# Performance work log

Hardware: AMD Instinct MI355X
Metric: run time of the kernel (lower is better)

Reference implementation:

```python
import jax, jax.numpy as jnp
import numpy as np

D_MODEL = 1024
N_HEADS = 16
HEAD_DIM = D_MODEL // N_HEADS
THETA = 10000.0
B, S = 4, 2048


def setup_inputs() -> dict:
    key = jax.random.key(0)
    ks = jax.random.split(key, 5)
    scale = 1.0 / np.sqrt(D_MODEL)
    x = jax.random.normal(ks[0], (B, S, D_MODEL), dtype=jnp.float32)
    token_positions = jnp.broadcast_to(jnp.arange(S, dtype=jnp.int32)[None, :], (B, S))
    WQ = jax.random.normal(ks[1], (D_MODEL, D_MODEL), dtype=jnp.float32) * scale
    WK = jax.random.normal(ks[2], (D_MODEL, D_MODEL), dtype=jnp.float32) * scale
    WV = jax.random.normal(ks[3], (D_MODEL, D_MODEL), dtype=jnp.float32) * scale
    WO = jax.random.normal(ks[4], (D_MODEL, D_MODEL), dtype=jnp.float32) * scale
    return {"x": x, "token_positions": token_positions, "WQ": WQ, "WK": WK, "WV": WV, "WO": WO}


def _apply_rope(t, token_positions):
    # t: [b, h, s, d]; token_positions: [b, s]
    d = t.shape[-1]
    inv_freq = THETA ** (-jnp.arange(0, d, 2, dtype=jnp.float32) / d)  # [d/2]
    ang = token_positions.astype(jnp.float32)[:, None, :, None] * inv_freq  # [b,1,s,d/2]
    cos, sin = jnp.cos(ang), jnp.sin(ang)
    t_even, t_odd = t[..., 0::2], t[..., 1::2]
    r_even = t_even * cos - t_odd * sin
    r_odd = t_even * sin + t_odd * cos
    out = jnp.stack([r_even, r_odd], axis=-1)  # interleave pairs back
    return out.reshape(t.shape)


def reference(x, token_positions, WQ, WK, WV, WO):
    b, s, _ = x.shape
    def proj(W):
        y = jnp.einsum('bsd,ed->bse', x, W)  # Linear: x @ W^T, W is [out,in]
        return y.reshape(b, s, N_HEADS, HEAD_DIM).transpose(0, 2, 1, 3)  # [b,h,s,d]
    Q = _apply_rope(proj(WQ), token_positions)
    K = _apply_rope(proj(WK), token_positions)
    V = proj(WV)
    scores = jnp.einsum('bhqd,bhkd->bhqk', Q, K) / jnp.sqrt(jnp.float32(HEAD_DIM))
    causal = jnp.tril(jnp.ones((s, s), dtype=bool))
    scores = jnp.where(causal, scores, -jnp.inf)
    attn = jax.nn.softmax(scores, axis=-1)
    out = jnp.einsum('bhqk,bhkd->bhqd', attn, V)
    out = out.transpose(0, 2, 1, 3).reshape(b, s, D_MODEL)
    return jnp.einsum('bse,oe->bso', out, WO)
```

## Files before the change

kernel.cpp:

```cpp
#include <hip/hip_runtime.h>

typedef __bf16 bf16x8 __attribute__((ext_vector_type(8)));
typedef __bf16 bf16x2 __attribute__((ext_vector_type(2)));
typedef float f32x4 __attribute__((ext_vector_type(4)));
typedef unsigned short u16;
typedef unsigned int u32;

#define MFMA16(a, b, c) __builtin_amdgcn_mfma_f32_16x16x32_bf16((a), (b), (c), 0, 0, 0)

__device__ __forceinline__ u16 f2b(float f) {
  u32 u = __float_as_uint(f);
  u += 0x7FFFu + ((u >> 16) & 1u);
  return (u16)(u >> 16);
}
__device__ __forceinline__ float b2f(u16 h) { return __uint_as_float(((u32)h) << 16); }

__device__ __forceinline__ u32 pkbf(float a, float b) {
  bf16x2 h = {(__bf16)a, (__bf16)b};
  return __builtin_bit_cast(u32, h);
}

__device__ __forceinline__ float exp2_(float x) {
#if __has_builtin(__builtin_amdgcn_exp2f)
  return __builtin_amdgcn_exp2f(x);
#else
  return exp2f(x);
#endif
}

__device__ __forceinline__ void glds16(const void* g, void* l) {
  __builtin_amdgcn_global_load_lds((const __attribute__((address_space(1))) void*)g,
                                   (__attribute__((address_space(3))) void*)l, 16, 0, 0);
}

__global__ __launch_bounds__(256) void cvt_k(const float* __restrict__ x,
                                             const float* __restrict__ wq,
                                             const float* __restrict__ wk,
                                             const float* __restrict__ wv,
                                             const float* __restrict__ wo,
                                             u16* __restrict__ dst) {
  size_t e = ((size_t)blockIdx.x * 256 + threadIdx.x) * 4;
  const float* src;
  size_t off;
  if (e < 8388608ull) {
    src = x; off = e;
  } else {
    size_t r = e - 8388608ull;
    u32 wi = (u32)(r >> 20);
    off = r & 1048575ull;
    src = (wi == 0) ? wq : (wi == 1) ? wk : (wi == 2) ? wv : wo;
  }
  float4 v = *(const float4*)(src + off);
  ushort4 o = make_ushort4(f2b(v.x), f2b(v.y), f2b(v.z), f2b(v.w));
  *(ushort4*)(dst + e) = o;
}

__global__ __launch_bounds__(256) void rope_tab_k(const int* __restrict__ pos,
                                                  float2* __restrict__ tab) {
  int i = blockIdx.x * 256 + threadIdx.x;
  int row = i >> 5, j = i & 31;
  float p = (float)pos[row];
  float inv = exp2f((float)j * -0.41524101186092029f);
  float s, c;
  sincosf(p * inv, &s, &c);
  tab[i] = make_float2(c, s);
}

__global__ __launch_bounds__(512, 2) void gemm_qkv_k(const u16* __restrict__ Xb,
                                                     const u16* __restrict__ Wq,
                                                     const u16* __restrict__ Wk,
                                                     const u16* __restrict__ Wv,
                                                     const float2* __restrict__ tab,
                                                     u16* __restrict__ Qp,
                                                     u16* __restrict__ Kp,
                                                     u16* __restrict__ Vt) {
  __shared__ u16 As[3][16384];
  __shared__ u16 Bs[3][8192];
  const int wgid = blockIdx.x;
  const int xcd = wgid & 7;
  const int idx = wgid >> 3;
  const int P = xcd * 12 + (idx >> 3);
  const int nt = idx & 7;
  const int z = P >> 5;
  const int mt = P & 31;
  const u16* W = (z == 0) ? Wq : (z == 1) ? Wk : Wv;
  const int t = threadIdx.x;
  const int wave = t >> 6, lane = t & 63;
  const int lr = lane & 15, lg = lane >> 4;
  const int wr = wave >> 1, wc = wave & 1;

  const int srow = t >> 3;
  const int scc = t & 7;
  const int ssw = scc ^ (srow & 7);
  const u16* aA = Xb + (size_t)(mt * 256 + srow) * 1024 + ssw * 8;
  const u16* bB = W + (size_t)(nt * 128 + srow) * 1024 + ssw * 8;

  f32x4 acc[4][4];
#pragma unroll
  for (int i = 0; i < 4; ++i)
#pragma unroll
    for (int j = 0; j < 4; ++j) acc[i][j] = (f32x4){0.f, 0.f, 0.f, 0.f};

#pragma unroll
  for (int tt = 0; tt < 2; ++tt) {
    const int kt = tt * 64;
    glds16(aA + kt, &As[tt][t * 8]);
    glds16(aA + 64 * 1024 + kt, &As[tt][4096 + t * 8]);
    glds16(bB + kt, &Bs[tt][t * 8]);
    glds16(aA + 128 * 1024 + kt, &As[tt][8192 + t * 8]);
    glds16(aA + 192 * 1024 + kt, &As[tt][12288 + t * 8]);
    glds16(bB + 64 * 1024 + kt, &Bs[tt][4096 + t * 8]);
  }
  asm volatile("s_waitcnt vmcnt(6)" ::: "memory");
  __builtin_amdgcn_s_barrier();

  const int arow = (wr * 64 + lr) * 64;
  const int brow = (wc * 64 + lr) * 64;
  const int sw = lr & 7;

  int sl = 0;
  for (int tau = 0; tau < 16; ++tau) {
    const int sp2 = (sl + 2 >= 3) ? sl - 1 : sl + 2;
    const u16* Asl = &As[sl][0];
    const u16* Bsl = &Bs[sl][0];
    u16* Ad = &As[sp2][0];
    u16* Bd = &Bs[sp2][0];
    const int kt2 = (tau + 2) * 64;
    bf16x8 af[4], bf[4];

    {
      const int koff = (lg ^ sw) * 8;
#pragma unroll
      for (int mi = 0; mi < 4; ++mi)
        af[mi] = *(const bf16x8*)&Asl[arow + mi * 1024 + koff];
#pragma unroll
      for (int nj = 0; nj < 4; ++nj)
        bf[nj] = *(const bf16x8*)&Bsl[brow + nj * 1024 + koff];
    }
    if (tau < 14) {
      glds16(aA + kt2, &Ad[t * 8]);
      glds16(aA + 64 * 1024 + kt2, &Ad[4096 + t * 8]);
      glds16(bB + kt2, &Bd[t * 8]);
    }
    __builtin_amdgcn_s_barrier();
    asm volatile("s_waitcnt lgkmcnt(0)" ::: "memory");
    __builtin_amdgcn_sched_barrier(0);
    __builtin_amdgcn_s_setprio(1);
#pragma unroll
    for (int mi = 0; mi < 4; ++mi)
#pragma unroll
      for (int nj = 0; nj < 4; ++nj)
        acc[mi][nj] = MFMA16(af[mi], bf[nj], acc[mi][nj]);
    __builtin_amdgcn_s_setprio(0);
    __builtin_amdgcn_sched_barrier(0);
    __builtin_amdgcn_s_barrier();

    {
      const int koff = ((4 + lg) ^ sw) * 8;
#pragma unroll
      for (int mi = 0; mi < 4; ++mi)
        af[mi] = *(const bf16x8*)&Asl[arow + mi * 1024 + koff];
#pragma unroll
      for (int nj = 0; nj < 4; ++nj)
        bf[nj] = *(const bf16x8*)&Bsl[brow + nj * 1024 + koff];
    }
    if (tau < 14) {
      glds16(aA + 128 * 1024 + kt2, &Ad[8192 + t * 8]);
      glds16(aA + 192 * 1024 + kt2, &Ad[12288 + t * 8]);
      glds16(bB + 64 * 1024 + kt2, &Bd[4096 + t * 8]);
    }
    __builtin_amdgcn_s_barrier();
    asm volatile("s_waitcnt lgkmcnt(0)" ::: "memory");
    __builtin_amdgcn_sched_barrier(0);
    __builtin_amdgcn_s_setprio(1);
#pragma unroll
    for (int mi = 0; mi < 4; ++mi)
#pragma unroll
      for (int nj = 0; nj < 4; ++nj)
        acc[mi][nj] = MFMA16(af[mi], bf[nj], acc[mi][nj]);
    __builtin_amdgcn_s_setprio(0);
    __builtin_amdgcn_sched_barrier(0);
    if (tau < 14) asm volatile("s_waitcnt vmcnt(6)" ::: "memory");
    else asm volatile("s_waitcnt vmcnt(0)" ::: "memory");
    __builtin_amdgcn_s_barrier();
    sl = (sl == 2) ? 0 : sl + 1;
  }

  const int rbase = mt * 256 + wr * 64 + lg * 4;
  const int cbase = nt * 128 + wc * 64 + lr;
  if (z < 2) {
    u16* out = (z == 0) ? Qp : Kp;
    const float scl = (z == 0) ? 0.18033688011112043f : 1.0f;
#pragma unroll
    for (int mi = 0; mi < 4; ++mi)
#pragma unroll
      for (int nj = 0; nj < 4; ++nj) {
        int row0 = rbase + mi * 16;
        int col = cbase + nj * 16;
        int j = (col >> 1) & 31;
        float sgn = (col & 1) ? 1.f : -1.f;
#pragma unroll
        for (int r = 0; r < 4; ++r) {
          float self = acc[mi][nj][r];
          float partner = __shfl_xor(self, 1);
          float2 cs = tab[(size_t)(row0 + r) * 32 + j];
          float o = (self * cs.x + partner * cs.y * sgn) * scl;
          out[(size_t)(row0 + r) * 1024 + col] = f2b(o);
        }
      }
  } else {
#pragma unroll
    for (int mi = 0; mi < 4; ++mi)
#pragma unroll
      for (int nj = 0; nj < 4; ++nj) {
        int row0 = rbase + mi * 16;
        int e = cbase + nj * 16;
        int b = row0 >> 11, s = row0 & 2047;
        ushort4 pk = make_ushort4(f2b(acc[mi][nj][0]), f2b(acc[mi][nj][1]),
                                  f2b(acc[mi][nj][2]), f2b(acc[mi][nj][3]));
        *(ushort4*)&Vt[((size_t)(b * 1024 + e)) * 2048 + s] = pk;
      }
  }
}

__global__ __launch_bounds__(256) void fattn_k(const u16* __restrict__ Qp,
                                               const u16* __restrict__ Kp,
                                               const u16* __restrict__ Vt,
                                               u16* __restrict__ Ao) {
  __shared__ u16 Ks[2][64 * 64];
  __shared__ u16 Vs[2][64 * 64];
  __shared__ u16 Ps[4][32 * 64];
  const int blk = blockIdx.x;
  const int g = blk & 7, jj = blk >> 3;
  const int bh = g * 8 + (jj & 7);
  const int qt = 15 - (jj >> 3);
  const int b = bh >> 4, h = bh & 15;
  const int tid = threadIdx.x, wave = tid >> 6, lane = tid & 63;
  const int lr = lane & 15, lg = lane >> 4;
  const int q0w = qt * 128 + wave * 32;

  bf16x8 qf[2][2];
#pragma unroll
  for (int qh = 0; qh < 2; ++qh) {
    const u16* qb = Qp + ((size_t)(b * 2048 + q0w + qh * 16 + lr)) * 1024 + h * 64 + lg * 8;
    qf[qh][0] = *(const bf16x8*)qb;
    qf[qh][1] = *(const bf16x8*)(qb + 32);
  }

  float m[2], l[2];
  f32x4 oacc[2][4];
#pragma unroll
  for (int qh = 0; qh < 2; ++qh) {
    m[qh] = -1e30f; l[qh] = 0.f;
#pragma unroll
    for (int d4 = 0; d4 < 4; ++d4) oacc[qh][d4] = (f32x4){0.f, 0.f, 0.f, 0.f};
  }

  const int srow = lane >> 3;
  const int schunk = (lane & 7) ^ srow;
  const u16* kbase = Kp + ((size_t)(b * 2048 + 16 * wave + srow)) * 1024 + h * 64 + schunk * 8;
  const u16* vbase = Vt + ((size_t)(b * 1024 + h * 64 + 16 * wave + srow)) * 2048 + schunk * 8;
  char* psbase = (char*)&Ps[wave][0];

  const int ktmax = 2 * qt + 1;
  const int ktmask = q0w >> 6;
  const int ktneed = 2 * qt + (wave >> 1);

  glds16(kbase, &Ks[0][(16 * wave) * 64]);
  glds16(kbase + 8192, &Ks[0][(16 * wave + 8) * 64]);
  glds16(vbase, &Vs[0][(16 * wave) * 64]);
  glds16(vbase + 16384, &Vs[0][(16 * wave + 8) * 64]);

  int cur = 0;
  for (int kt = 0; kt <= ktmax; ++kt, cur ^= 1) {
    __syncthreads();
    if (kt < ktmax) {
      const int nx = cur ^ 1, k1 = kt + 1;
      glds16(kbase + (size_t)k1 * 65536, &Ks[nx][(16 * wave) * 64]);
      glds16(kbase + (size_t)k1 * 65536 + 8192, &Ks[nx][(16 * wave + 8) * 64]);
      glds16(vbase + k1 * 64, &Vs[nx][(16 * wave) * 64]);
      glds16(vbase + k1 * 64 + 16384, &Vs[nx][(16 * wave + 8) * 64]);
    }
    if (kt > ktneed) continue;
    const u16* KB = &Ks[cur][0];
    const u16* VB = &Vs[cur][0];

    f32x4 sc[2][4];
#pragma unroll
    for (int ks = 0; ks < 4; ++ks) {
      const int krow = ks * 16 + lr;
      const int sw = lr & 7;
      bf16x8 kf0 = *(const bf16x8*)&KB[krow * 64 + ((lg ^ sw) * 8)];
      bf16x8 kf1 = *(const bf16x8*)&KB[krow * 64 + (((lg + 4) ^ sw) * 8)];
#pragma unroll
      for (int qh = 0; qh < 2; ++qh) {
        f32x4 s = (f32x4){0.f, 0.f, 0.f, 0.f};
        s = MFMA16(kf0, qf[qh][0], s);
        s = MFMA16(kf1, qf[qh][1], s);
        sc[qh][ks] = s;
      }
    }
    if (kt >= ktmask) {
#pragma unroll
      for (int qh = 0; qh < 2; ++qh) {
        int q = q0w + qh * 16 + lr;
#pragma unroll
        for (int ks = 0; ks < 4; ++ks)
#pragma unroll
          for (int r = 0; r < 4; ++r) {
            int kv = kt * 64 + ks * 16 + lg * 4 + r;
            if (kv > q) sc[qh][ks][r] = -__builtin_inff();
          }
      }
    }

#pragma unroll
    for (int qh = 0; qh < 2; ++qh) {
      float pm = sc[qh][0][0];
#pragma unroll
      for (int ks = 0; ks < 4; ++ks)
#pragma unroll
        for (int r = 0; r < 4; ++r) pm = fmaxf(pm, sc[qh][ks][r]);
      pm = fmaxf(pm, __shfl_xor(pm, 16));
      pm = fmaxf(pm, __shfl_xor(pm, 32));
      if (__any(pm > m[qh] + 8.f)) {
        float mn = fmaxf(m[qh], pm);
        float corr = exp2_(m[qh] - mn);
        m[qh] = mn;
        l[qh] *= corr;
        float cb[4];
#pragma unroll
        for (int r = 0; r < 4; ++r) cb[r] = __shfl(corr, (lane & 48) | (lg * 4 + r));
#pragma unroll
        for (int d4 = 0; d4 < 4; ++d4)
#pragma unroll
          for (int r = 0; r < 4; ++r) oacc[qh][d4][r] *= cb[r];
      }
      float rs = 0.f;
#pragma unroll
      for (int ks = 0; ks < 4; ++ks)
#pragma unroll
        for (int r = 0; r < 4; ++r) {
          float p = exp2_(sc[qh][ks][r] - m[qh]);
          sc[qh][ks][r] = p;
          rs += p;
        }
      rs += __shfl_xor(rs, 16);
      rs += __shfl_xor(rs, 32);
      l[qh] += rs;
    }

#pragma unroll
    for (int qh = 0; qh < 2; ++qh) {
      const int row = qh * 16 + lr;
      const int sw = lr & 7;
#pragma unroll
      for (int ks = 0; ks < 4; ++ks) {
        const int chunk = (2 * ks + (lg >> 1)) ^ sw;
        char* p = psbase + row * 128 + chunk * 16 + (lg & 1) * 8;
        *(uint2*)p = make_uint2(pkbf(sc[qh][ks][0], sc[qh][ks][1]),
                                pkbf(sc[qh][ks][2], sc[qh][ks][3]));
      }
    }
    bf16x8 pa[2][2];
#pragma unroll
    for (int qh = 0; qh < 2; ++qh) {
      const int row = qh * 16 + lr;
      const int sw = lr & 7;
      pa[qh][0] = *(const bf16x8*)(psbase + row * 128 + ((lg ^ sw) * 16));
      pa[qh][1] = *(const bf16x8*)(psbase + row * 128 + (((lg + 4) ^ sw) * 16));
    }
#pragma unroll
    for (int d4 = 0; d4 < 4; ++d4) {
      const int vrow = d4 * 16 + lr;
      const int sw = lr & 7;
      bf16x8 vf0 = *(const bf16x8*)&VB[vrow * 64 + ((lg ^ sw) * 8)];
      bf16x8 vf1 = *(const bf16x8*)&VB[vrow * 64 + (((lg + 4) ^ sw) * 8)];
      oacc[0][d4] = MFMA16(pa[0][0], vf0, oacc[0][d4]);
      oacc[0][d4] = MFMA16(pa[0][1], vf1, oacc[0][d4]);
      oacc[1][d4] = MFMA16(pa[1][0], vf0, oacc[1][d4]);
      oacc[1][d4] = MFMA16(pa[1][1], vf1, oacc[1][d4]);
    }
  }

#pragma unroll
  for (int qh = 0; qh < 2; ++qh) {
    float lb[4];
#pragma unroll
    for (int r = 0; r < 4; ++r) lb[r] = __shfl(l[qh], (lane & 48) | (lg * 4 + r));
#pragma unroll
    for (int r = 0; r < 4; ++r) {
      float inv = 1.f / lb[r];
      int q = q0w + qh * 16 + lg * 4 + r;
      u16* orow = Ao + ((size_t)(b * 2048 + q)) * 1024 + h * 64 + lr;
#pragma unroll
      for (int d4 = 0; d4 < 4; ++d4) orow[d4 * 16] = f2b(oacc[qh][d4][r] * inv);
    }
  }
}

__global__ __launch_bounds__(256) void gemm_wo_k(const u16* __restrict__ Ab,
                                                 const u16* __restrict__ Wo,
                                                 float* __restrict__ Out) {
  __shared__ u16 As[128 * 32];
  __shared__ u16 Bs[128 * 32];
  const int wgid = blockIdx.x;
  const int xcd = wgid & 7;
  const int idx = wgid >> 3;
  const int mt = xcd * 8 + (idx >> 3);
  const int nt = idx & 7;
  const int tid = threadIdx.x, wave = tid >> 6, lane = tid & 63;
  const int wr = (wave >> 1) * 64, wc = (wave & 1) * 64;
  const int lr = lane & 15, lg = lane >> 4;
  const size_t arow = (size_t)(mt * 128 + wave * 32 + (lane >> 2)) * 1024 + (lane & 3) * 8;
  const size_t brow = (size_t)(nt * 128 + wave * 32 + (lane >> 2)) * 1024 + (lane & 3) * 8;
  u16* Ad0 = &As[(wave * 32) * 32];
  u16* Ad1 = &As[(wave * 32 + 16) * 32];
  u16* Bd0 = &Bs[(wave * 32) * 32];
  u16* Bd1 = &Bs[(wave * 32 + 16) * 32];

  f32x4 acc[4][4];
#pragma unroll
  for (int i = 0; i < 4; ++i)
#pragma unroll
    for (int j = 0; j < 4; ++j) acc[i][j] = (f32x4){0.f, 0.f, 0.f, 0.f};

  for (int kt = 0; kt < 1024; kt += 32) {
    glds16(Ab + arow + kt, Ad0);
    glds16(Ab + arow + kt + 16 * 1024, Ad1);
    glds16(Wo + brow + kt, Bd0);
    glds16(Wo + brow + kt + 16 * 1024, Bd1);
    __syncthreads();
    bf16x8 af[4], bfr[4];
#pragma unroll
    for (int mi = 0; mi < 4; ++mi)
      af[mi] = *(const bf16x8*)&As[(wr + mi * 16 + lr) * 32 + lg * 8];
#pragma unroll
    for (int ni = 0; ni < 4; ++ni)
      bfr[ni] = *(const bf16x8*)&Bs[(wc + ni * 16 + lr) * 32 + lg * 8];
#pragma unroll
    for (int mi = 0; mi < 4; ++mi)
#pragma unroll
      for (int ni = 0; ni < 4; ++ni)
        acc[mi][ni] = MFMA16(af[mi], bfr[ni], acc[mi][ni]);
    __syncthreads();
  }
#pragma unroll
  for (int mi = 0; mi < 4; ++mi)
#pragma unroll
    for (int ni = 0; ni < 4; ++ni) {
      int row0 = mt * 128 + wr + mi * 16 + lg * 4;
      int col = nt * 128 + wc + ni * 16 + lr;
#pragma unroll
      for (int r = 0; r < 4; ++r)
        Out[(size_t)(row0 + r) * 1024 + col] = acc[mi][ni][r];
    }
}

extern "C" void kernel_launch(void* const* d_in, const int* in_sizes, int n_in,
                              void* d_out, int out_size, void* d_ws, size_t ws_size,
                              hipStream_t stream) {
  const float* x = (const float*)d_in[0];
  const int* pos = (const int*)d_in[1];
  const float* wq = (const float*)d_in[2];
  const float* wk = (const float*)d_in[3];
  const float* wv = (const float*)d_in[4];
  const float* wo = (const float*)d_in[5];

  char* ws = (char*)d_ws;
  u16* xb = (u16*)ws;
  u16* wqb = xb + 8388608;
  u16* wkb = wqb + 1048576;
  u16* wvb = wkb + 1048576;
  u16* wob = wvb + 1048576;
  float2* tab = (float2*)(ws + 25165824);
  u16* Qp = (u16*)(ws + 27262976);
  u16* Kp = (u16*)(ws + 27262976 + 16777216);
  u16* Vt = (u16*)(ws + 27262976 + 2 * 16777216);
  u16* Ao = (u16*)(ws + 27262976 + 3 * 16777216);

  hipLaunchKernelGGL(cvt_k, dim3(12288), dim3(256), 0, stream, x, wq, wk, wv, wo, xb);
  hipLaunchKernelGGL(rope_tab_k, dim3(1024), dim3(256), 0, stream, pos, tab);
  hipLaunchKernelGGL(gemm_qkv_k, dim3(768), dim3(512), 0, stream, xb, wqb, wkb, wvb,
                     tab, Qp, Kp, Vt);
  hipLaunchKernelGGL(fattn_k, dim3(1024), dim3(256), 0, stream, Qp, Kp, Vt, Ao);
  hipLaunchKernelGGL(gemm_wo_k, dim3(512), dim3(256), 0, stream, Ao, wob, (float*)d_out);
}
```

Before: 188.4 us.

## Pipeline WO GEMM with triple-buffered LDS and tweak attention softmax math

Rewrites the output-projection GEMM to use 256x128 tiles with 512 threads, a 64-wide K step and a triple-buffered LDS pipeline. Global-to-LDS loads for later stages are issued while MFMAs run, and the kernel uses explicit waitcnt/barrier scheduling and setprio. In attention, the row max now uses v_max3 and the exp/sum uses paired float2 ops. The aim is to hide memory latency in the WO GEMM and trim ALU work in softmax, at the cost of more LDS per block and fragile hand-written synchronization.

Measured after the change: 183.4 us. -2.6%, faster.

```diff
diff --git a/kernel.cpp b/kernel.cpp
--- a/kernel.cpp
+++ b/kernel.cpp
@@ -3,6 +3,7 @@
 typedef __bf16 bf16x8 __attribute__((ext_vector_type(8)));
 typedef __bf16 bf16x2 __attribute__((ext_vector_type(2)));
 typedef float f32x4 __attribute__((ext_vector_type(4)));
+typedef float f32x2 __attribute__((ext_vector_type(2)));
 typedef unsigned short u16;
 typedef unsigned int u32;
 
@@ -18,6 +19,12 @@
 __device__ __forceinline__ u32 pkbf(float a, float b) {
   bf16x2 h = {(__bf16)a, (__bf16)b};
   return __builtin_bit_cast(u32, h);
+}
+
+__device__ __forceinline__ float max3f(float a, float b, float c) {
+  float d;
+  asm("v_max3_f32 %0, %1, %2, %3" : "=v"(d) : "v"(a), "v"(b), "v"(c));
+  return d;
 }
 
 __device__ __forceinline__ float exp2_(float x) {
@@ -255,6 +262,7 @@
 #pragma unroll
     for (int d4 = 0; d4 < 4; ++d4) oacc[qh][d4] = (f32x4){0.f, 0.f, 0.f, 0.f};
   }
+  const f32x4 fz = {0.f, 0.f, 0.f, 0.f};
 
   const int srow = lane >> 3;
   const int schunk = (lane & 7) ^ srow;
@@ -289,13 +297,12 @@
 #pragma unroll
     for (int ks = 0; ks < 4; ++ks) {
       const int krow = ks * 16 + lr;
-      const int sw = lr & 7;
-      bf16x8 kf0 = *(const bf16x8*)&KB[krow * 64 + ((lg ^ sw) * 8)];
-      bf16x8 kf1 = *(const bf16x8*)&KB[krow * 64 + (((lg + 4) ^ sw) * 8)];
+      const int swk = lr & 7;
+      bf16x8 kf0 = *(const bf16x8*)&KB[krow * 64 + ((lg ^ swk) * 8)];
+      bf16x8 kf1 = *(const bf16x8*)&KB[krow * 64 + (((lg + 4) ^ swk) * 8)];
 #pragma unroll
       for (int qh = 0; qh < 2; ++qh) {
-        f32x4 s = (f32x4){0.f, 0.f, 0.f, 0.f};
-        s = MFMA16(kf0, qf[qh][0], s);
+        f32x4 s = MFMA16(kf0, qf[qh][0], fz);
         s = MFMA16(kf1, qf[qh][1], s);
         sc[qh][ks] = s;
       }
@@ -316,11 +323,13 @@
 
 #pragma unroll
     for (int qh = 0; qh < 2; ++qh) {
-      float pm = sc[qh][0][0];
-#pragma unroll
-      for (int ks = 0; ks < 4; ++ks)
-#pragma unroll
-        for (int r = 0; r < 4; ++r) pm = fmaxf(pm, sc[qh][ks][r]);
+      float t0 = max3f(sc[qh][0][0], sc[qh][0][1], sc[qh][0][2]);
+      float t1 = max3f(sc[qh][0][3], sc[qh][1][0], sc[qh][1][1]);
+      float t2 = max3f(sc[qh][1][2], sc[qh][1][3], sc[qh][2][0]);
+      float t3 = max3f(sc[qh][2][1], sc[qh][2][2], sc[qh][2][3]);
+      float t4 = max3f(sc[qh][3][0], sc[qh][3][1], sc[qh][3][2]);
+      float pm = max3f(max3f(t0, t1, t2), max3f(t3, t4, sc[qh][3][3]),
+                       -1e30f);
       pm = fmaxf(pm, __shfl_xor(pm, 16));
       pm = fmaxf(pm, __shfl_xor(pm, 32));
       if (__any(pm > m[qh] + 8.f)) {
@@ -336,15 +345,22 @@
 #pragma unroll
           for (int r = 0; r < 4; ++r) oacc[qh][d4][r] *= cb[r];
       }
-      float rs = 0.f;
-#pragma unroll
-      for (int ks = 0; ks < 4; ++ks)
-#pragma unroll
-        for (int r = 0; r < 4; ++r) {
-          float p = exp2_(sc[qh][ks][r] - m[qh]);
-          sc[qh][ks][r] = p;
-          rs += p;
-        }
+      const f32x2 ms = {m[qh], m[qh]};
+      f32x2 rs2 = {0.f, 0.f};
+#pragma unroll
+      for (int ks = 0; ks < 4; ++ks) {
+        f32x2 lo = {sc[qh][ks][0], sc[qh][ks][1]};
+        f32x2 hi = {sc[qh][ks][2], sc[qh][ks][3]};
+        lo = lo - ms;
+        hi = hi - ms;
+        lo[0] = exp2_(lo[0]); lo[1] = exp2_(lo[1]);
+        hi[0] = exp2_(hi[0]); hi[1] = exp2_(hi[1]);
+        rs2 += lo;
+        rs2 += hi;
+        sc[qh][ks][0] = lo[0]; sc[qh][ks][1] = lo[1];
+        sc[qh][ks][2] = hi[0]; sc[qh][ks][3] = hi[1];
+      }
+      float rs = rs2[0] + rs2[1];
       rs += __shfl_xor(rs, 16);
       rs += __shfl_xor(rs, 32);
       l[qh] += rs;
@@ -353,10 +369,10 @@
 #pragma unroll
     for (int qh = 0; qh < 2; ++qh) {
       const int row = qh * 16 + lr;
-      const int sw = lr & 7;
+      const int swp = lr & 7;
 #pragma unroll
       for (int ks = 0; ks < 4; ++ks) {
-        const int chunk = (2 * ks + (lg >> 1)) ^ sw;
+        const int chunk = (2 * ks + (lg >> 1)) ^ swp;
         char* p = psbase + row * 128 + chunk * 16 + (lg & 1) * 8;
         *(uint2*)p = make_uint2(pkbf(sc[qh][ks][0], sc[qh][ks][1]),
                                 pkbf(sc[qh][ks][2], sc[qh][ks][3]));
@@ -366,16 +382,16 @@
 #pragma unroll
     for (int qh = 0; qh < 2; ++qh) {
       const int row = qh * 16 + lr;
-      const int sw = lr & 7;
-      pa[qh][0] = *(const bf16x8*)(psbase + row * 128 + ((lg ^ sw) * 16));
-      pa[qh][1] = *(const bf16x8*)(psbase + row * 128 + (((lg + 4) ^ sw) * 16));
+      const int swp = lr & 7;
+      pa[qh][0] = *(const bf16x8*)(psbase + row * 128 + ((lg ^ swp) * 16));
+      pa[qh][1] = *(const bf16x8*)(psbase + row * 128 + (((lg + 4) ^ swp) * 16));
     }
 #pragma unroll
     for (int d4 = 0; d4 < 4; ++d4) {
       const int vrow = d4 * 16 + lr;
-      const int sw = lr & 7;
-      bf16x8 vf0 = *(const bf16x8*)&VB[vrow * 64 + ((lg ^ sw) * 8)];
-      bf16x8 vf1 = *(const bf16x8*)&VB[vrow * 64 + (((lg + 4) ^ sw) * 8)];
+      const int swv = lr & 7;
+      bf16x8 vf0 = *(const bf16x8*)&VB[vrow * 64 + ((lg ^ swv) * 8)];
+      bf16x8 vf1 = *(const bf16x8*)&VB[vrow * 64 + (((lg + 4) ^ swv) * 8)];
       oacc[0][d4] = MFMA16(pa[0][0], vf0, oacc[0][d4]);
       oacc[0][d4] = MFMA16(pa[0][1], vf1, oacc[0][d4]);
       oacc[1][d4] = MFMA16(pa[1][0], vf0, oacc[1][d4]);
@@ -399,25 +415,26 @@
   }
 }
 
-__global__ __launch_bounds__(256) void gemm_wo_k(const u16* __restrict__ Ab,
-                                                 const u16* __restrict__ Wo,
-                                                 float* __restrict__ Out) {
-  __shared__ u16 As[128 * 32];
-  __shared__ u16 Bs[128 * 32];
+__global__ __launch_bounds__(512, 2) void gemm_wo_k(const u16* __restrict__ Ab,
+                                                    const u16* __restrict__ Wo,
+                                                    float* __restrict__ Out) {
+  __shared__ u16 As[3][16384];
+  __shared__ u16 Bs[3][8192];
   const int wgid = blockIdx.x;
   const int xcd = wgid & 7;
   const int idx = wgid >> 3;
-  const int mt = xcd * 8 + (idx >> 3);
+  const int mt = xcd * 4 + (idx >> 3);
   const int nt = idx & 7;
-  const int tid = threadIdx.x, wave = tid >> 6, lane = tid & 63;
-  const int wr = (wave >> 1) * 64, wc = (wave & 1) * 64;
+  const int t = threadIdx.x;
+  const int wave = t >> 6, lane = t & 63;
   const int lr = lane & 15, lg = lane >> 4;
-  const size_t arow = (size_t)(mt * 128 + wave * 32 + (lane >> 2)) * 1024 + (lane & 3) * 8;
-  const size_t brow = (size_t)(nt * 128 + wave * 32 + (lane >> 2)) * 1024 + (lane & 3) * 8;
-  u16* Ad0 = &As[(wave * 32) * 32];
-  u16* Ad1 = &As[(wave * 32 + 16) * 32];
-  u16* Bd0 = &Bs[(wave * 32) * 32];
-  u16* Bd1 = &Bs[(wave * 32 + 16) * 32];
+  const int wr = wave >> 1, wc = wave & 1;
+
+  const int srow = t >> 3;
+  const int scc = t & 7;
+  const int ssw = scc ^ (srow & 7);
+  const u16* aA = Ab + (size_t)(mt * 256 + srow) * 1024 + ssw * 8;
+  const u16* bB = Wo + (size_t)(nt * 128 + srow) * 1024 + ssw * 8;
 
   f32x4 acc[4][4];
 #pragma unroll
@@ -425,35 +442,102 @@
 #pragma unroll
     for (int j = 0; j < 4; ++j) acc[i][j] = (f32x4){0.f, 0.f, 0.f, 0.f};
 
-  for (int kt = 0; kt < 1024; kt += 32) {
-    glds16(Ab + arow + kt, Ad0);
-    glds16(Ab + arow + kt + 16 * 1024, Ad1);
-    glds16(Wo + brow + kt, Bd0);
-    glds16(Wo + brow + kt + 16 * 1024, Bd1);
-    __syncthreads();
-    bf16x8 af[4], bfr[4];
+#pragma unroll
+  for (int tt = 0; tt < 2; ++tt) {
+    const int kt = tt * 64;
+    glds16(aA + kt, &As[tt][t * 8]);
+    glds16(aA + 64 * 1024 + kt, &As[tt][4096 + t * 8]);
+    glds16(bB + kt, &Bs[tt][t * 8]);
+    glds16(aA + 128 * 1024 + kt, &As[tt][8192 + t * 8]);
+    glds16(aA + 192 * 1024 + kt, &As[tt][12288 + t * 8]);
+    glds16(bB + 64 * 1024 + kt, &Bs[tt][4096 + t * 8]);
+  }
+  asm volatile("s_waitcnt vmcnt(6)" ::: "memory");
+  __builtin_amdgcn_s_barrier();
+
+  const int arow = (wr * 64 + lr) * 64;
+  const int brow = (wc * 64 + lr) * 64;
+  const int sw = lr & 7;
+
+  int sl = 0;
+  for (int tau = 0; tau < 16; ++tau) {
+    const int sp2 = (sl + 2 >= 3) ? sl - 1 : sl + 2;
+    const u16* Asl = &As[sl][0];
+    const u16* Bsl = &Bs[sl][0];
+    u16* Ad = &As[sp2][0];
+    u16* Bd = &Bs[sp2][0];
+    const int kt2 = (tau + 2) * 64;
+    bf16x8 af[4], bf[4];
+
+    {
+      const int koff = (lg ^ sw) * 8;
+#pragma unroll
+      for (int mi = 0; mi < 4; ++mi)
+        af[mi] = *(const bf16x8*)&Asl[arow + mi * 1024 + koff];
+#pragma unroll
+      for (int nj = 0; nj < 4; ++nj)
+        bf[nj] = *(const bf16x8*)&Bsl[brow + nj * 1024 + koff];
+    }
+    if (tau < 14) {
+      glds16(aA + kt2, &Ad[t * 8]);
+      glds16(aA + 64 * 1024 + kt2, &Ad[4096 + t * 8]);
+      glds16(bB + kt2, &Bd[t * 8]);
+    }
+    __builtin_amdgcn_s_barrier();
+    asm volatile("s_waitcnt lgkmcnt(0)" ::: "memory");
+    __builtin_amdgcn_sched_barrier(0);
+    __builtin_amdgcn_s_setprio(1);
 #pragma unroll
     for (int mi = 0; mi < 4; ++mi)
-      af[mi] = *(const bf16x8*)&As[(wr + mi * 16 + lr) * 32 + lg * 8];
-#pragma unroll
-    for (int ni = 0; ni < 4; ++ni)
-      bfr[ni] = *(const bf16x8*)&Bs[(wc + ni * 16 + lr) * 32 + lg * 8];
+#pragma unroll
+      for (int nj = 0; nj < 4; ++nj)
+        acc[mi][nj] = MFMA16(af[mi], bf[nj], acc[mi][nj]);
+    __builtin_amdgcn_s_setprio(0);
+    __builtin_amdgcn_sched_barrier(0);
+    __builtin_amdgcn_s_barrier();
+
+    {
+      const int koff = ((4 + lg) ^ sw) * 8;
+#pragma unroll
+      for (int mi = 0; mi < 4; ++mi)
+        af[mi] = *(const bf16x8*)&Asl[arow + mi * 1024 + koff];
+#pragma unroll
+      for (int nj = 0; nj < 4; ++nj)
+        bf[nj] = *(const bf16x8*)&Bsl[brow + nj * 1024 + koff];
+    }
+    if (tau < 14) {
+      glds16(aA + 128 * 1024 + kt2, &Ad[8192 + t * 8]);
+      glds16(aA + 192 * 1024 + kt2, &Ad[12288 + t * 8]);
+      glds16(bB + 64 * 1024 + kt2, &Bd[4096 + t * 8]);
+    }
+    __builtin_amdgcn_s_barrier();
+    asm volatile("s_waitcnt lgkmcnt(0)" ::: "memory");
+    __builtin_amdgcn_sched_barrier(0);
+    __builtin_amdgcn_s_setprio(1);
 #pragma unroll
     for (int mi = 0; mi < 4; ++mi)
 #pragma unroll
-      for (int ni = 0; ni < 4; ++ni)
-        acc[mi][ni] = MFMA16(af[mi], bfr[ni], acc[mi][ni]);
-    __syncthreads();
-  }
+      for (int nj = 0; nj < 4; ++nj)
+        acc[mi][nj] = MFMA16(af[mi], bf[nj], acc[mi][nj]);
+    __builtin_amdgcn_s_setprio(0);
+    __builtin_amdgcn_sched_barrier(0);
+    if (tau < 14) asm volatile("s_waitcnt vmcnt(6)" ::: "memory");
+    else asm volatile("s_waitcnt vmcnt(0)" ::: "memory");
+    __builtin_amdgcn_s_barrier();
+    sl = (sl == 2) ? 0 : sl + 1;
+  }
+
+  const int rbase = mt * 256 + wr * 64 + lg * 4;
+  const int cbase = nt * 128 + wc * 64 + lr;
 #pragma unroll
   for (int mi = 0; mi < 4; ++mi)
 #pragma unroll
-    for (int ni = 0; ni < 4; ++ni) {
-      int row0 = mt * 128 + wr + mi * 16 + lg * 4;
-      int col = nt * 128 + wc + ni * 16 + lr;
+    for (int nj = 0; nj < 4; ++nj) {
+      int row0 = rbase + mi * 16;
+      int col = cbase + nj * 16;
 #pragma unroll
       for (int r = 0; r < 4; ++r)
-        Out[(size_t)(row0 + r) * 1024 + col] = acc[mi][ni][r];
+        Out[(size_t)(row0 + r) * 1024 + col] = acc[mi][nj][r];
     }
 }
 
@@ -484,5 +568,5 @@
   hipLaunchKernelGGL(gemm_qkv_k, dim3(768), dim3(512), 0, stream, xb, wqb, wkb, wvb,
                      tab, Qp, Kp, Vt);
   hipLaunchKernelGGL(fattn_k, dim3(1024), dim3(256), 0, stream, Qp, Kp, Vt, Ao);
-  hipLaunchKernelGGL(gemm_wo_k, dim3(512), dim3(256), 0, stream, Ao, wob, (float*)d_out);
-}
+  hipLaunchKernelGGL(gemm_wo_k, dim3(256), dim3(512), 0, stream, Ao, wob, (float*)d_out);
+}
```
